# Optimization experiments

Hardware: AMD Instinct MI355X
Metric: run time of the kernel (lower is better)

The kernel has to match this reference:

```python
import jax, jax.numpy as jnp
import numpy as np

N = 20000      # nodes
E = 160000     # edges (before self loops)
IN = 128       # in_channels (== edge_dim)
H = 8          # heads
C = 64         # out_channels per head
NEG_SLOPE = 0.2


def setup_inputs() -> dict:
    key = jax.random.key(0)
    ks = jax.random.split(key, 8)
    s_in = np.float32(1.0 / np.sqrt(IN))
    s_att = np.float32(1.0 / np.sqrt(C))
    return {
        "x": jax.random.normal(ks[0], (N, IN), jnp.float32),
        "edge_index": jax.random.randint(ks[1], (2, E), 0, N, dtype=jnp.int32),
        "edge_attr": jax.random.normal(ks[2], (E, IN), jnp.float32),
        "Wl": jax.random.normal(ks[3], (IN, H * C), jnp.float32) * s_in,
        "Wr": jax.random.normal(ks[4], (IN, H * C), jnp.float32) * s_in,
        "We": jax.random.normal(ks[5], (IN, H * C), jnp.float32) * s_in,
        "att": jax.random.normal(ks[6], (H, C), jnp.float32) * s_att,
        "bias": jnp.zeros((H * C,), jnp.float32),
    }


def reference(x, edge_index, edge_attr, Wl, Wr, We, att, bias):
    n = x.shape[0]
    e = edge_attr.shape[0]
    src, dst = edge_index[0], edge_index[1]

    # add self loops; self-loop edge_attr = per-target-node mean of incoming
    # edge attrs (PyG fill_value='mean'); nodes with no in-edges get zeros.
    cnt = jax.ops.segment_sum(jnp.ones((e,), x.dtype), dst, num_segments=n)
    loop_attr = jax.ops.segment_sum(edge_attr, dst, num_segments=n) / jnp.maximum(cnt, 1.0)[:, None]
    loops = jnp.arange(n, dtype=src.dtype)
    src_f = jnp.concatenate([src, loops])          # [E+N]
    dst_f = jnp.concatenate([dst, loops])          # [E+N]
    ea = jnp.concatenate([edge_attr, loop_attr], axis=0)  # [E+N, IN]

    xl = (x @ Wl).reshape(n, H, C)   # source projection
    xr = (x @ Wr).reshape(n, H, C)   # target projection
    xe = (ea @ We).reshape(-1, H, C)  # edge projection

    # GATv2 score: att . LeakyReLU(xl_j + xr_i + xe)
    m = jax.nn.leaky_relu(xl[src_f] + xr[dst_f] + xe, NEG_SLOPE)  # [E+N, H, C]
    logits = jnp.einsum('ehc,hc->eh', m, att)                      # [E+N, H]

    # segment softmax over incoming edges of each target node
    lmax = jax.ops.segment_max(logits, dst_f, num_segments=n)      # [N, H]
    p = jnp.exp(logits - lmax[dst_f])
    denom = jax.ops.segment_sum(p, dst_f, num_segments=n)
    alpha = p / denom[dst_f]                                       # [E+N, H]

    # weighted scatter-add aggregation of source features
    out = jax.ops.segment_sum(alpha[:, :, None] * xl[src_f], dst_f, num_segments=n)
    return out.reshape(n, H * C) + bias
```

## Files before the change

kernel.cpp:

```cpp
#include <hip/hip_runtime.h>

#define N_NODES 20000
#define E_EDGES 160000
#define IN_CH 128
#define H_HEADS 8
#define C_CH 64
#define HC 512
#define M_TOT (E_EDGES + N_NODES)
#define NEG_SLOPE 0.2f
#define NCHUNK ((N_NODES + 255) / 256)

typedef __attribute__((ext_vector_type(8))) short bf16x8;
typedef __attribute__((ext_vector_type(4))) float f32x4;

__device__ __forceinline__ unsigned short f2bf(float f) {
    unsigned u = __float_as_uint(f);
    unsigned r = (u + 0x7FFFu + ((u >> 16) & 1u)) >> 16;
    return (unsigned short)r;
}
__device__ __forceinline__ unsigned short f2bf_trunc(float f) {
    return (unsigned short)(__float_as_uint(f) >> 16);
}
__device__ __forceinline__ float bf2f(unsigned short s) {
    return __uint_as_float((unsigned)s << 16);
}
__device__ __forceinline__ float bfx(const bf16x8& v0, const bf16x8& v1, int idx) {
    return bf2f((unsigned short)((idx < 8) ? v0[idx] : v1[idx - 8]));
}
__device__ __forceinline__ void agg8(float* ac, const bf16x8& v, float alpha) {
    #pragma unroll
    for (int jj = 0; jj < 8; ++jj) ac[jj] = fmaf(alpha, bf2f((unsigned short)v[jj]), ac[jj]);
}

#define GLOAD_LDS16(gsrc, ldst) \
    __builtin_amdgcn_global_load_lds((const __attribute__((address_space(1))) void*)(gsrc), \
                                     (__attribute__((address_space(3))) void*)(ldst), 16, 0, 0)

__global__ void k_deg(const int* __restrict__ ei, int* __restrict__ deg) {
    int e = blockIdx.x * blockDim.x + threadIdx.x;
    if (e >= E_EDGES) return;
    atomicAdd(&deg[ei[E_EDGES + e]], 1);
}

__global__ void k_scan1(const int* __restrict__ deg, int* __restrict__ bsum) {
    __shared__ int red[256];
    int tid = threadIdx.x;
    int i = blockIdx.x * 256 + tid;
    red[tid] = (i < N_NODES) ? deg[i] + 1 : 0;
    __syncthreads();
    for (int off = 128; off > 0; off >>= 1) {
        if (tid < off) red[tid] += red[tid + off];
        __syncthreads();
    }
    if (tid == 0) bsum[blockIdx.x] = red[0];
}

__global__ void k_scan2(const int* __restrict__ bsum, int* __restrict__ boff) {
    if (threadIdx.x == 0) {
        int run = 0;
        for (int b = 0; b < NCHUNK; ++b) { boff[b] = run; run += bsum[b]; }
    }
}

__global__ void k_scan3(const int* __restrict__ deg, const int* __restrict__ boff,
                        int* __restrict__ rowptr, int* __restrict__ cursor,
                        int4* __restrict__ edat) {
    __shared__ int buf[256];
    int tid = threadIdx.x;
    int i = blockIdx.x * 256 + tid;
    int v = (i < N_NODES) ? deg[i] + 1 : 0;
    buf[tid] = v;
    __syncthreads();
    for (int off = 1; off < 256; off <<= 1) {
        int tv = (tid >= off) ? buf[tid - off] : 0;
        __syncthreads();
        buf[tid] += tv;
        __syncthreads();
    }
    if (i < N_NODES) {
        int excl = boff[blockIdx.x] + buf[tid] - v;
        rowptr[i] = excl;
        edat[excl] = make_int4(E_EDGES + i, i, i, 0);
        cursor[i] = excl + 1;
        if (i == N_NODES - 1) rowptr[N_NODES] = excl + v;
    }
}

__global__ void k_fill(const int* __restrict__ ei, int* __restrict__ cursor,
                       int4* __restrict__ edat) {
    int e = blockIdx.x * blockDim.x + threadIdx.x;
    if (e >= E_EDGES) return;
    int d = ei[E_EDGES + e];
    int slot = atomicAdd(&cursor[d], 1);
    edat[slot] = make_int4(e, ei[e], d, 0);
}

__global__ void k_prep(const int* __restrict__ rowptr, const int4* __restrict__ edat,
                       const float* __restrict__ ea, unsigned short* __restrict__ eab) {
    int node = (blockIdx.x * blockDim.x + threadIdx.x) >> 6;
    int lane = threadIdx.x & 63;
    if (node >= N_NODES) return;
    int beg = rowptr[node] + 1, end = rowptr[node + 1];
    int len = end - beg;
    float s0 = 0.f, s1 = 0.f;
    float a0 = 0, b0 = 0, a1 = 0, b1 = 0, a2 = 0, b2 = 0, a3 = 0, b3 = 0;
    const float* P;
    if (0 < len) { P = ea + (size_t)edat[beg + 0].x * 128 + lane; a0 = P[0]; b0 = P[64]; }
    if (1 < len) { P = ea + (size_t)edat[beg + 1].x * 128 + lane; a1 = P[0]; b1 = P[64]; }
    if (2 < len) { P = ea + (size_t)edat[beg + 2].x * 128 + lane; a2 = P[0]; b2 = P[64]; }
    if (3 < len) { P = ea + (size_t)edat[beg + 3].x * 128 + lane; a3 = P[0]; b3 = P[64]; }
    int j = 0;
    #define PREP_STEP(A, B) { \
        s0 += A; s1 += B; \
        eab[(size_t)(beg + j) * 128 + lane] = f2bf(A); \
        eab[(size_t)(beg + j) * 128 + 64 + lane] = f2bf(B); \
        if (j + 4 < len) { P = ea + (size_t)edat[beg + j + 4].x * 128 + lane; A = P[0]; B = P[64]; } \
        ++j; }
    for (; j + 4 <= len; ) {
        PREP_STEP(a0, b0);
        PREP_STEP(a1, b1);
        PREP_STEP(a2, b2);
        PREP_STEP(a3, b3);
    }
    if (j < len) { s0 += a0; s1 += b0; eab[(size_t)(beg + j) * 128 + lane] = f2bf(a0); eab[(size_t)(beg + j) * 128 + 64 + lane] = f2bf(b0); ++j; }
    if (j < len) { s0 += a1; s1 += b1; eab[(size_t)(beg + j) * 128 + lane] = f2bf(a1); eab[(size_t)(beg + j) * 128 + 64 + lane] = f2bf(b1); ++j; }
    if (j < len) { s0 += a2; s1 += b2; eab[(size_t)(beg + j) * 128 + lane] = f2bf(a2); eab[(size_t)(beg + j) * 128 + 64 + lane] = f2bf(b2); ++j; }
    #undef PREP_STEP
    float inv = 1.f / fmaxf((float)len, 1.f);
    eab[(size_t)(beg - 1) * 128 + lane] = f2bf(s0 * inv);
    eab[(size_t)(beg - 1) * 128 + 64 + lane] = f2bf(s1 * inv);
}

__global__ void k_trans3(const float* __restrict__ Wl, const float* __restrict__ Wr,
                         const float* __restrict__ We,
                         unsigned short* __restrict__ WlT, unsigned short* __restrict__ WrT,
                         unsigned short* __restrict__ WeT) {
    int idx = blockIdx.x * blockDim.x + threadIdx.x;
    if (idx >= HC * IN_CH) return;
    int m = blockIdx.y;
    const float* W = (m == 0) ? Wl : (m == 1) ? Wr : We;
    unsigned short* WT = (m == 0) ? WlT : (m == 1) ? WrT : WeT;
    int n = idx >> 7, k = idx & 127;
    WT[idx] = f2bf(W[(size_t)k * HC + n]);
}

__global__ void k_gemm2(const float* __restrict__ A,
                        const unsigned short* __restrict__ WlT,
                        const unsigned short* __restrict__ WrT,
                        unsigned short* __restrict__ xlb, unsigned short* __restrict__ xrb,
                        int M) {
    __shared__ short As[64 * 128];
    int row0 = blockIdx.x * 64;
    int sel = blockIdx.y >> 1;
    const unsigned short* BT = sel ? WrT : WlT;
    unsigned short* Cb = sel ? xrb : xlb;
    int t = threadIdx.x;
    {
        int row = t >> 2, c0 = (t & 3) * 32;
        int gr = row0 + row;
        int sw = (row & 7) << 4;
        const float* src = A + (size_t)gr * 128 + c0;
        #pragma unroll
        for (int i = 0; i < 4; ++i) {
            bf16x8 v;
            if (gr < M) {
                const float4* p = (const float4*)(src + i * 8);
                float4 f0 = p[0], f1 = p[1];
                v[0] = f2bf(f0.x); v[1] = f2bf(f0.y); v[2] = f2bf(f0.z); v[3] = f2bf(f0.w);
                v[4] = f2bf(f1.x); v[5] = f2bf(f1.y); v[6] = f2bf(f1.z); v[7] = f2bf(f1.w);
            } else {
                #pragma unroll
                for (int j = 0; j < 8; ++j) v[j] = 0;
            }
            int off = row * 256 + (((c0 + i * 8) * 2) ^ sw);
            *(bf16x8*)((char*)As + off) = v;
        }
    }
    __syncthreads();

    int w = t >> 6, l = t & 63;
    int lr = l & 15, lk = l >> 4;
    int col0 = (blockIdx.y & 1) * 256 + w * 64;

    f32x4 acc[4][4];
    #pragma unroll
    for (int mi = 0; mi < 4; ++mi)
        #pragma unroll
        for (int fj = 0; fj < 4; ++fj)
            #pragma unroll
            for (int q = 0; q < 4; ++q) acc[mi][fj][q] = 0.f;

    #pragma unroll
    for (int k0 = 0; k0 < 4; ++k0) {
        bf16x8 a4[4];
        #pragma unroll
        for (int mi = 0; mi < 4; ++mi) {
            int row = mi * 16 + lr;
            int off = row * 256 + ((k0 * 64 + lk * 16) ^ ((row & 7) << 4));
            a4[mi] = *(const bf16x8*)((const char*)As + off);
        }
        #pragma unroll
        for (int fj = 0; fj < 4; ++fj) {
            bf16x8 b = *(const bf16x8*)(BT + (size_t)(col0 + fj * 16 + lr) * 128 + k0 * 32 + lk * 8);
            #pragma unroll
            for (int mi = 0; mi < 4; ++mi)
                acc[mi][fj] = __builtin_amdgcn_mfma_f32_16x16x32_bf16(a4[mi], b, acc[mi][fj], 0, 0, 0);
        }
    }
    #pragma unroll
    for (int mi = 0; mi < 4; ++mi) {
        #pragma unroll
        for (int reg = 0; reg < 4; ++reg) {
            int r = row0 + mi * 16 + lk * 4 + reg;
            if (r < M) {
                unsigned short* cp = Cb + (size_t)r * 512 + col0 + lr;
                #pragma unroll
                for (int fj = 0; fj < 4; ++fj) cp[fj * 16] = f2bf(acc[mi][fj][reg]);
            }
        }
    }
}

#define PREF(R, CB, SLOT) { \
    int s_ = s_src[R], d_ = s_dst[R]; \
    const bf16x8* xp_ = (const bf16x8*)(xlb + (size_t)s_ * 512 + (CB) + q * 16); \
    pa0[SLOT] = xp_[0]; pa1[SLOT] = xp_[1]; \
    const bf16x8* rp_ = (const bf16x8*)(xrb + (size_t)d_ * 512 + (CB) + q * 16); \
    pb0[SLOT] = rp_[0]; pb1[SLOT] = rp_[1]; }

__global__ __launch_bounds__(512, 2)
void k_fused(const int4* __restrict__ edat, const int* __restrict__ rowptr,
             const unsigned short* __restrict__ eab,
             const unsigned short* __restrict__ WeT,
             const unsigned short* __restrict__ xlb,
             const unsigned short* __restrict__ xrb,
             const float* __restrict__ att, const float* __restrict__ bias,
             float* __restrict__ logits, float* __restrict__ out) {
    __shared__ short As[64 * 128];
    __shared__ unsigned short xeT[8][16][72];
    __shared__ float att_s[512];
    __shared__ float lg[64][8];
    __shared__ int s_src[64], s_dst[64];
    __shared__ int own_node[64], own_beg[64], own_len[64];
    __shared__ int n_own;
    int row0 = blockIdx.x * 64;
    int t = threadIdx.x;

    if (t == 0) n_own = 0;
    __syncthreads();

    {
        int l = t & 63;
        int c_base = (t >> 6) * 2;
        #pragma unroll
        for (int i = 0; i < 2; ++i) {
            int c = c_base + i;
            int row_local = c * 4 + (l >> 4);
            int grow = row0 + row_local;
            if (grow > M_TOT - 1) grow = M_TOT - 1;
            int chunk = (l & 15) ^ (row_local & 7);
            const char* src = (const char*)eab + (size_t)grow * 256 + chunk * 16;
            char* dst = (char*)As + c * 1024;
            GLOAD_LDS16(src, dst);
        }
    }

    if (t < 64) {
        int p = row0 + t;
        int s = 0, d = 0;
        if (p < M_TOT) {
            int4 v = edat[p];
            s = v.y; d = v.z;
            int pb = rowptr[d], pe = rowptr[d + 1];
            if (pb == p && pe <= row0 + 64) {
                int idx = atomicAdd(&n_own, 1);
                own_node[idx] = d; own_beg[idx] = t; own_len[idx] = pe - pb;
            }
        }
        s_src[t] = s; s_dst[t] = d;
    }
    att_s[t] = att[t];

    asm volatile("s_waitcnt vmcnt(0)");
    __syncthreads();

    int w = t >> 6, l = t & 63;
    int lr = l & 15, lk = l >> 4;
    int eloc = l >> 2, q = l & 3;
    int cb = w * 64;

    bf16x8 pa0[2], pa1[2], pb0[2], pb1[2];
    f32x4 acc[4][4];

    PREF(eloc, cb, 0);

    #pragma unroll
    for (int mi = 0; mi < 4; ++mi)
        #pragma unroll
        for (int fj = 0; fj < 4; ++fj)
            #pragma unroll
            for (int qq = 0; qq < 4; ++qq) acc[mi][fj][qq] = 0.f;

    #pragma unroll
    for (int k0 = 0; k0 < 4; ++k0) {
        bf16x8 a4[4];
        #pragma unroll
        for (int mi = 0; mi < 4; ++mi) {
            int row = mi * 16 + lr;
            int off = row * 256 + ((k0 * 64 + lk * 16) ^ ((row & 7) << 4));
            a4[mi] = *(const bf16x8*)((const char*)As + off);
        }
        #pragma unroll
        for (int fj = 0; fj < 4; ++fj) {
            bf16x8 b = *(const bf16x8*)(WeT + (size_t)(cb + fj * 16 + lr) * 128 + k0 * 32 + lk * 8);
            #pragma unroll
            for (int mi = 0; mi < 4; ++mi)
                acc[mi][fj] = __builtin_amdgcn_mfma_f32_16x16x32_bf16(a4[mi], b, acc[mi][fj], 0, 0, 0);
        }
    }

    #pragma unroll
    for (int mi = 0; mi < 4; ++mi) {
        if (mi < 3) { PREF(mi * 16 + 16 + eloc, cb, (mi + 1) & 1); }

        #pragma unroll
        for (int fj = 0; fj < 4; ++fj)
            #pragma unroll
            for (int reg = 0; reg < 4; ++reg)
                xeT[w][lk * 4 + reg][fj * 16 + lr] = f2bf_trunc(acc[mi][fj][reg]);

        const bf16x8 ca0 = pa0[mi & 1], ca1 = pa1[mi & 1];
        const bf16x8 cb0v = pb0[mi & 1], cb1v = pb1[mi & 1];

        bf16x8 x0 = *(const bf16x8*)&xeT[w][eloc][q * 16];
        bf16x8 x1 = *(const bf16x8*)&xeT[w][eloc][q * 16 + 8];

        float sum = 0.f;
        #pragma unroll
        for (int sg = 0; sg < 4; ++sg) {
            float4 av = *(const float4*)&att_s[cb + q * 16 + sg * 4];
            float v0 = bfx(x0, x1, sg * 4 + 0) + bfx(ca0, ca1, sg * 4 + 0) + bfx(cb0v, cb1v, sg * 4 + 0);
            float v1 = bfx(x0, x1, sg * 4 + 1) + bfx(ca0, ca1, sg * 4 + 1) + bfx(cb0v, cb1v, sg * 4 + 1);
            float v2 = bfx(x0, x1, sg * 4 + 2) + bfx(ca0, ca1, sg * 4 + 2) + bfx(cb0v, cb1v, sg * 4 + 2);
            float v3 = bfx(x0, x1, sg * 4 + 3) + bfx(ca0, ca1, sg * 4 + 3) + bfx(cb0v, cb1v, sg * 4 + 3);
            v0 = (v0 > 0.f) ? v0 : v0 * NEG_SLOPE;
            v1 = (v1 > 0.f) ? v1 : v1 * NEG_SLOPE;
            v2 = (v2 > 0.f) ? v2 : v2 * NEG_SLOPE;
            v3 = (v3 > 0.f) ? v3 : v3 * NEG_SLOPE;
            sum = fmaf(av.x, v0, sum);
            sum = fmaf(av.y, v1, sum);
            sum = fmaf(av.z, v2, sum);
            sum = fmaf(av.w, v3, sum);
        }
        sum += __shfl_xor(sum, 1, 64);
        sum += __shfl_xor(sum, 2, 64);
        if (q == 0) lg[mi * 16 + eloc][w] = sum;
    }
    __syncthreads();

    {
        int nval = (M_TOT - row0 < 64 ? M_TOT - row0 : 64) * 8;
        if (t < 256 && t * 2 < nval) {
            const float* lf = (const float*)lg;
            float2 v = { lf[t * 2], lf[t * 2 + 1] };
            *(float2*)(logits + (size_t)row0 * 8 + t * 2) = v;
        }
    }

    {
        int lane = t & 63;
        int h = lane >> 3;
        for (int o = w; o < n_own; o += 8) {
            int d = own_node[o], rb = own_beg[o], len = own_len[o];
            float m = -3.4e38f;
            for (int j = 0; j < len; ++j) m = fmaxf(m, lg[rb + j][h]);
            float den = 0.f;
            for (int j = 0; j < len; ++j) den += __expf(lg[rb + j][h] - m);
            float rden = 1.f / den;
            float ac[8] = {};
            bf16x8 v0 = {}, v1 = {}, v2 = {}, v3 = {};
            if (0 < len) v0 = *(const bf16x8*)(xlb + (size_t)s_src[rb + 0] * 512 + lane * 8);
            if (1 < len) v1 = *(const bf16x8*)(xlb + (size_t)s_src[rb + 1] * 512 + lane * 8);
            if (2 < len) v2 = *(const bf16x8*)(xlb + (size_t)s_src[rb + 2] * 512 + lane * 8);
            if (3 < len) v3 = *(const bf16x8*)(xlb + (size_t)s_src[rb + 3] * 512 + lane * 8);
            int j = 0;
            #define AGG_STEP(V) { \
                agg8(ac, V, __expf(lg[rb + j][h] - m) * rden); \
                if (j + 4 < len) V = *(const bf16x8*)(xlb + (size_t)s_src[rb + j + 4] * 512 + lane * 8); \
                ++j; }
            for (; j + 4 <= len; ) {
                AGG_STEP(v0);
                AGG_STEP(v1);
                AGG_STEP(v2);
                AGG_STEP(v3);
            }
            if (j < len) { agg8(ac, v0, __expf(lg[rb + j][h] - m) * rden); ++j; }
            if (j < len) { agg8(ac, v1, __expf(lg[rb + j][h] - m) * rden); ++j; }
            if (j < len) { agg8(ac, v2, __expf(lg[rb + j][h] - m) * rden); ++j; }
            #undef AGG_STEP
            float4* op = (float4*)(out + (size_t)d * 512 + lane * 8);
            const float4* bp = (const float4*)(bias + lane * 8);
            float4 bv0 = bp[0], bv1 = bp[1];
            float4 r0 = { ac[0] + bv0.x, ac[1] + bv0.y, ac[2] + bv0.z, ac[3] + bv0.w };
            float4 r1 = { ac[4] + bv1.x, ac[5] + bv1.y, ac[6] + bv1.z, ac[7] + bv1.w };
            op[0] = r0; op[1] = r1;
        }
    }
}

__global__ void k_cleanup(const int* __restrict__ rowptr, const int4* __restrict__ edat,
                          const float* __restrict__ logits,
                          const unsigned short* __restrict__ xlb, const float* __restrict__ bias,
                          float* __restrict__ out) {
    int node = (blockIdx.x * blockDim.x + threadIdx.x) >> 6;
    int lane = threadIdx.x & 63;
    if (node >= N_NODES) return;
    int beg = rowptr[node], end = rowptr[node + 1];
    if ((beg >> 6) == ((end - 1) >> 6)) return;
    int h = lane >> 3;
    int len = end - beg;

    float m = -3.4e38f;
    for (int p = beg; p < end; ++p) m = fmaxf(m, logits[(size_t)p * 8 + h]);
    float den = 0.f;
    for (int p = beg; p < end; ++p) den += __expf(logits[(size_t)p * 8 + h] - m);
    float rden = 1.f / den;

    float acc[8] = {};
    bf16x8 v0 = {}, v1 = {}, v2 = {}, v3 = {};
    if (0 < len) v0 = *(const bf16x8*)(xlb + (size_t)edat[beg + 0].y * 512 + lane * 8);
    if (1 < len) v1 = *(const bf16x8*)(xlb + (size_t)edat[beg + 1].y * 512 + lane * 8);
    if (2 < len) v2 = *(const bf16x8*)(xlb + (size_t)edat[beg + 2].y * 512 + lane * 8);
    if (3 < len) v3 = *(const bf16x8*)(xlb + (size_t)edat[beg + 3].y * 512 + lane * 8);
    int j = 0;
    #define CLN_STEP(V) { \
        agg8(acc, V, __expf(logits[(size_t)(beg + j) * 8 + h] - m) * rden); \
        if (j + 4 < len) V = *(const bf16x8*)(xlb + (size_t)edat[beg + j + 4].y * 512 + lane * 8); \
        ++j; }
    for (; j + 4 <= len; ) {
        CLN_STEP(v0);
        CLN_STEP(v1);
        CLN_STEP(v2);
        CLN_STEP(v3);
    }
    if (j < len) { agg8(acc, v0, __expf(logits[(size_t)(beg + j) * 8 + h] - m) * rden); ++j; }
    if (j < len) { agg8(acc, v1, __expf(logits[(size_t)(beg + j) * 8 + h] - m) * rden); ++j; }
    if (j < len) { agg8(acc, v2, __expf(logits[(size_t)(beg + j) * 8 + h] - m) * rden); ++j; }
    #undef CLN_STEP
    float4* op = (float4*)(out + (size_t)node * 512 + lane * 8);
    const float4* bp = (const float4*)(bias + lane * 8);
    float4 bv0 = bp[0], bv1 = bp[1];
    float4 r0 = { acc[0] + bv0.x, acc[1] + bv0.y, acc[2] + bv0.z, acc[3] + bv0.w };
    float4 r1 = { acc[4] + bv1.x, acc[5] + bv1.y, acc[6] + bv1.z, acc[7] + bv1.w };
    op[0] = r0; op[1] = r1;
}

extern "C" void kernel_launch(void* const* d_in, const int* in_sizes, int n_in,
                              void* d_out, int out_size, void* d_ws, size_t ws_size,
                              hipStream_t stream) {
    const float* x    = (const float*)d_in[0];
    const int*   ei   = (const int*)d_in[1];
    const float* ea   = (const float*)d_in[2];
    const float* Wl   = (const float*)d_in[3];
    const float* Wr   = (const float*)d_in[4];
    const float* We   = (const float*)d_in[5];
    const float* att  = (const float*)d_in[6];
    const float* bias = (const float*)d_in[7];
    float* out = (float*)d_out;

    unsigned short* xlb = (unsigned short*)d_ws;
    unsigned short* xrb = xlb + (size_t)N_NODES * HC;
    unsigned short* WlT = xrb + (size_t)N_NODES * HC;
    unsigned short* WrT = WlT + HC * IN_CH;
    unsigned short* WeT = WrT + HC * IN_CH;
    unsigned short* eab = WeT + HC * IN_CH;
    float* logits    = (float*)(eab + (size_t)M_TOT * IN_CH);
    int4* edat       = (int4*)(logits + (size_t)M_TOT * 8);
    int* deg         = (int*)(edat + M_TOT);
    int* rowptr      = deg + N_NODES;
    int* cursor      = rowptr + N_NODES + 1;
    int* bsum        = cursor + N_NODES;
    int* boff        = bsum + NCHUNK;

    const int B = 256;
    hipMemsetAsync(deg, 0, N_NODES * sizeof(int), stream);
    k_deg<<<(E_EDGES + B - 1) / B, B, 0, stream>>>(ei, deg);
    k_scan1<<<NCHUNK, B, 0, stream>>>(deg, bsum);
    k_scan2<<<1, 64, 0, stream>>>(bsum, boff);
    k_scan3<<<NCHUNK, B, 0, stream>>>(deg, boff, rowptr, cursor, edat);
    k_fill<<<(E_EDGES + B - 1) / B, B, 0, stream>>>(ei, cursor, edat);
    k_prep<<<((size_t)N_NODES * 64 + B - 1) / B, B, 0, stream>>>(rowptr, edat, ea, eab);
    k_trans3<<<dim3((HC * IN_CH + B - 1) / B, 3), B, 0, stream>>>(Wl, Wr, We, WlT, WrT, WeT);
    k_gemm2<<<dim3((N_NODES + 63) / 64, 4), B, 0, stream>>>(x, WlT, WrT, xlb, xrb, N_NODES);
    k_fused<<<(M_TOT + 63) / 64, 512, 0, stream>>>(edat, rowptr, eab, WeT,
                                                   xlb, xrb, att, bias, logits, out);
    k_cleanup<<<((size_t)N_NODES * 64 + B - 1) / B, B, 0, stream>>>(rowptr, edat, logits,
                                                                    xlb, bias, out);
}
```

Measured before the change: 221.1 us.

## Halve MFMA accumulator footprint, raise occupancy, and remap aggregation to head-per-wave

The edge-projection MFMA now runs in two halves of 32 rows, so only 2x4 accumulator tiles are live at once, and launch bounds ask for 4 blocks per SM instead of 2. The aim is lower register pressure and more resident waves to hide gather latency. The owned-node aggregation changes from one wave per node with 8 channels per lane to every wave handling every node for its own head, one channel per lane. That removes per-lane softmax redundancy across heads but swaps 16-byte vector gathers for 2-byte scalar loads, and each node's softmax is now computed once per wave.

```diff
diff --git a/kernel.cpp b/kernel.cpp
--- a/kernel.cpp
+++ b/kernel.cpp
@@ -228,7 +228,7 @@
     const bf16x8* rp_ = (const bf16x8*)(xrb + (size_t)d_ * 512 + (CB) + q * 16); \
     pb0[SLOT] = rp_[0]; pb1[SLOT] = rp_[1]; }
 
-__global__ __launch_bounds__(512, 2)
+__global__ __launch_bounds__(512, 4)
 void k_fused(const int4* __restrict__ edat, const int* __restrict__ rowptr,
              const unsigned short* __restrict__ eab,
              const unsigned short* __restrict__ WeT,
@@ -290,71 +290,75 @@
     int cb = w * 64;
 
     bf16x8 pa0[2], pa1[2], pb0[2], pb1[2];
-    f32x4 acc[4][4];
 
     PREF(eloc, cb, 0);
 
     #pragma unroll
-    for (int mi = 0; mi < 4; ++mi)
-        #pragma unroll
-        for (int fj = 0; fj < 4; ++fj)
-            #pragma unroll
-            for (int qq = 0; qq < 4; ++qq) acc[mi][fj][qq] = 0.f;
-
-    #pragma unroll
-    for (int k0 = 0; k0 < 4; ++k0) {
-        bf16x8 a4[4];
-        #pragma unroll
-        for (int mi = 0; mi < 4; ++mi) {
-            int row = mi * 16 + lr;
-            int off = row * 256 + ((k0 * 64 + lk * 16) ^ ((row & 7) << 4));
-            a4[mi] = *(const bf16x8*)((const char*)As + off);
-        }
-        #pragma unroll
-        for (int fj = 0; fj < 4; ++fj) {
-            bf16x8 b = *(const bf16x8*)(WeT + (size_t)(cb + fj * 16 + lr) * 128 + k0 * 32 + lk * 8);
-            #pragma unroll
-            for (int mi = 0; mi < 4; ++mi)
-                acc[mi][fj] = __builtin_amdgcn_mfma_f32_16x16x32_bf16(a4[mi], b, acc[mi][fj], 0, 0, 0);
-        }
-    }
-
-    #pragma unroll
-    for (int mi = 0; mi < 4; ++mi) {
-        if (mi < 3) { PREF(mi * 16 + 16 + eloc, cb, (mi + 1) & 1); }
-
-        #pragma unroll
-        for (int fj = 0; fj < 4; ++fj)
-            #pragma unroll
-            for (int reg = 0; reg < 4; ++reg)
-                xeT[w][lk * 4 + reg][fj * 16 + lr] = f2bf_trunc(acc[mi][fj][reg]);
-
-        const bf16x8 ca0 = pa0[mi & 1], ca1 = pa1[mi & 1];
-        const bf16x8 cb0v = pb0[mi & 1], cb1v = pb1[mi & 1];
-
-        bf16x8 x0 = *(const bf16x8*)&xeT[w][eloc][q * 16];
-        bf16x8 x1 = *(const bf16x8*)&xeT[w][eloc][q * 16 + 8];
-
-        float sum = 0.f;
-        #pragma unroll
-        for (int sg = 0; sg < 4; ++sg) {
-            float4 av = *(const float4*)&att_s[cb + q * 16 + sg * 4];
-            float v0 = bfx(x0, x1, sg * 4 + 0) + bfx(ca0, ca1, sg * 4 + 0) + bfx(cb0v, cb1v, sg * 4 + 0);
-            float v1 = bfx(x0, x1, sg * 4 + 1) + bfx(ca0, ca1, sg * 4 + 1) + bfx(cb0v, cb1v, sg * 4 + 1);
-            float v2 = bfx(x0, x1, sg * 4 + 2) + bfx(ca0, ca1, sg * 4 + 2) + bfx(cb0v, cb1v, sg * 4 + 2);
-            float v3 = bfx(x0, x1, sg * 4 + 3) + bfx(ca0, ca1, sg * 4 + 3) + bfx(cb0v, cb1v, sg * 4 + 3);
-            v0 = (v0 > 0.f) ? v0 : v0 * NEG_SLOPE;
-            v1 = (v1 > 0.f) ? v1 : v1 * NEG_SLOPE;
-            v2 = (v2 > 0.f) ? v2 : v2 * NEG_SLOPE;
-            v3 = (v3 > 0.f) ? v3 : v3 * NEG_SLOPE;
-            sum = fmaf(av.x, v0, sum);
-            sum = fmaf(av.y, v1, sum);
-            sum = fmaf(av.z, v2, sum);
-            sum = fmaf(av.w, v3, sum);
-        }
-        sum += __shfl_xor(sum, 1, 64);
-        sum += __shfl_xor(sum, 2, 64);
-        if (q == 0) lg[mi * 16 + eloc][w] = sum;
+    for (int mih = 0; mih < 2; ++mih) {
+        f32x4 acc[2][4];
+        #pragma unroll
+        for (int mi2 = 0; mi2 < 2; ++mi2)
+            #pragma unroll
+            for (int fj = 0; fj < 4; ++fj)
+                #pragma unroll
+                for (int qq = 0; qq < 4; ++qq) acc[mi2][fj][qq] = 0.f;
+
+        #pragma unroll
+        for (int k0 = 0; k0 < 4; ++k0) {
+            bf16x8 a4[2];
+            #pragma unroll
+            for (int mi2 = 0; mi2 < 2; ++mi2) {
+                int row = (mih * 2 + mi2) * 16 + lr;
+                int off = row * 256 + ((k0 * 64 + lk * 16) ^ ((row & 7) << 4));
+                a4[mi2] = *(const bf16x8*)((const char*)As + off);
+            }
+            #pragma unroll
+            for (int fj = 0; fj < 4; ++fj) {
+                bf16x8 b = *(const bf16x8*)(WeT + (size_t)(cb + fj * 16 + lr) * 128 + k0 * 32 + lk * 8);
+                #pragma unroll
+                for (int mi2 = 0; mi2 < 2; ++mi2)
+                    acc[mi2][fj] = __builtin_amdgcn_mfma_f32_16x16x32_bf16(a4[mi2], b, acc[mi2][fj], 0, 0, 0);
+            }
+        }
+
+        #pragma unroll
+        for (int mi2 = 0; mi2 < 2; ++mi2) {
+            int mi = mih * 2 + mi2;
+            if (mi < 3) { PREF(mi * 16 + 16 + eloc, cb, (mi + 1) & 1); }
+
+            #pragma unroll
+            for (int fj = 0; fj < 4; ++fj)
+                #pragma unroll
+                for (int reg = 0; reg < 4; ++reg)
+                    xeT[w][lk * 4 + reg][fj * 16 + lr] = f2bf_trunc(acc[mi2][fj][reg]);
+
+            const bf16x8 ca0 = pa0[mi & 1], ca1 = pa1[mi & 1];
+            const bf16x8 cb0v = pb0[mi & 1], cb1v = pb1[mi & 1];
+
+            bf16x8 x0 = *(const bf16x8*)&xeT[w][eloc][q * 16];
+            bf16x8 x1 = *(const bf16x8*)&xeT[w][eloc][q * 16 + 8];
+
+            float sum = 0.f;
+            #pragma unroll
+            for (int sg = 0; sg < 4; ++sg) {
+                float4 av = *(const float4*)&att_s[cb + q * 16 + sg * 4];
+                float v0 = bfx(x0, x1, sg * 4 + 0) + bfx(ca0, ca1, sg * 4 + 0) + bfx(cb0v, cb1v, sg * 4 + 0);
+                float v1 = bfx(x0, x1, sg * 4 + 1) + bfx(ca0, ca1, sg * 4 + 1) + bfx(cb0v, cb1v, sg * 4 + 1);
+                float v2 = bfx(x0, x1, sg * 4 + 2) + bfx(ca0, ca1, sg * 4 + 2) + bfx(cb0v, cb1v, sg * 4 + 2);
+                float v3 = bfx(x0, x1, sg * 4 + 3) + bfx(ca0, ca1, sg * 4 + 3) + bfx(cb0v, cb1v, sg * 4 + 3);
+                v0 = (v0 > 0.f) ? v0 : v0 * NEG_SLOPE;
+                v1 = (v1 > 0.f) ? v1 : v1 * NEG_SLOPE;
+                v2 = (v2 > 0.f) ? v2 : v2 * NEG_SLOPE;
+                v3 = (v3 > 0.f) ? v3 : v3 * NEG_SLOPE;
+                sum = fmaf(av.x, v0, sum);
+                sum = fmaf(av.y, v1, sum);
+                sum = fmaf(av.z, v2, sum);
+                sum = fmaf(av.w, v3, sum);
+            }
+            sum += __shfl_xor(sum, 1, 64);
+            sum += __shfl_xor(sum, 2, 64);
+            if (q == 0) lg[mi * 16 + eloc][w] = sum;
+        }
     }
     __syncthreads();
 
@@ -369,41 +373,36 @@
 
     {
         int lane = t & 63;
-        int h = lane >> 3;
-        for (int o = w; o < n_own; o += 8) {
+        float bv = bias[cb + lane];
+        for (int o = 0; o < n_own; ++o) {
             int d = own_node[o], rb = own_beg[o], len = own_len[o];
             float m = -3.4e38f;
-            for (int j = 0; j < len; ++j) m = fmaxf(m, lg[rb + j][h]);
+            for (int j = 0; j < len; ++j) m = fmaxf(m, lg[rb + j][w]);
             float den = 0.f;
-            for (int j = 0; j < len; ++j) den += __expf(lg[rb + j][h] - m);
+            for (int j = 0; j < len; ++j) den += __expf(lg[rb + j][w] - m);
             float rden = 1.f / den;
-            float ac[8] = {};
-            bf16x8 v0 = {}, v1 = {}, v2 = {}, v3 = {};
-            if (0 < len) v0 = *(const bf16x8*)(xlb + (size_t)s_src[rb + 0] * 512 + lane * 8);
-            if (1 < len) v1 = *(const bf16x8*)(xlb + (size_t)s_src[rb + 1] * 512 + lane * 8);
-            if (2 < len) v2 = *(const bf16x8*)(xlb + (size_t)s_src[rb + 2] * 512 + lane * 8);
-            if (3 < len) v3 = *(const bf16x8*)(xlb + (size_t)s_src[rb + 3] * 512 + lane * 8);
+            float ac = 0.f;
+            unsigned short x0 = 0, x1 = 0, x2 = 0, x3 = 0;
+            if (0 < len) x0 = xlb[(size_t)s_src[rb + 0] * 512 + cb + lane];
+            if (1 < len) x1 = xlb[(size_t)s_src[rb + 1] * 512 + cb + lane];
+            if (2 < len) x2 = xlb[(size_t)s_src[rb + 2] * 512 + cb + lane];
+            if (3 < len) x3 = xlb[(size_t)s_src[rb + 3] * 512 + cb + lane];
             int j = 0;
-            #define AGG_STEP(V) { \
-                agg8(ac, V, __expf(lg[rb + j][h] - m) * rden); \
-                if (j + 4 < len) V = *(const bf16x8*)(xlb + (size_t)s_src[rb + j + 4] * 512 + lane * 8); \
+            #define ASTEP(X) { \
+                ac = fmaf(__expf(lg[rb + j][w] - m) * rden, bf2f(X), ac); \
+                if (j + 4 < len) X = xlb[(size_t)s_src[rb + j + 4] * 512 + cb + lane]; \
                 ++j; }
             for (; j + 4 <= len; ) {
-                AGG_STEP(v0);
-                AGG_STEP(v1);
-                AGG_STEP(v2);
-                AGG_STEP(v3);
-            }
-            if (j < len) { agg8(ac, v0, __expf(lg[rb + j][h] - m) * rden); ++j; }
-            if (j < len) { agg8(ac, v1, __expf(lg[rb + j][h] - m) * rden); ++j; }
-            if (j < len) { agg8(ac, v2, __expf(lg[rb + j][h] - m) * rden); ++j; }
-            #undef AGG_STEP
-            float4* op = (float4*)(out + (size_t)d * 512 + lane * 8);
-            const float4* bp = (const float4*)(bias + lane * 8);
-            float4 bv0 = bp[0], bv1 = bp[1];
-            float4 r0 = { ac[0] + bv0.x, ac[1] + bv0.y, ac[2] + bv0.z, ac[3] + bv0.w };
-            float4 r1 = { ac[4] + bv1.x, ac[5] + bv1.y, ac[6] + bv1.z, ac[7] + bv1.w };
-            op[0] = r0; op[1] = r1;
+                ASTEP(x0);
+                ASTEP(x1);
+                ASTEP(x2);
+                ASTEP(x3);
+            }
+            if (j < len) { ac = fmaf(__expf(lg[rb + j][w] - m) * rden, bf2f(x0), ac); ++j; }
+            if (j < len) { ac = fmaf(__expf(lg[rb + j][w] - m) * rden, bf2f(x1), ac); ++j; }
+            if (j < len) { ac = fmaf(__expf(lg[rb + j][w] - m) * rden, bf2f(x2), ac); ++j; }
+            #undef ASTEP
+            out[(size_t)d * 512 + cb + lane] = ac + bv;
         }
     }
 }
```

After: 304.3 us. 37.6% more time.
